# Kernel optimization log

Measured on AMD Instinct MI355X. Metric: run time of the kernel, lower is better.

Reference implementation:

```python
import jax, jax.numpy as jnp
import numpy as np

N_NODES = 1_000_000
N_UPD = 200_000
D_MEM = 172
D_MSG = 172


def setup_inputs() -> dict:
    key = jax.random.key(0)
    ks = jax.random.split(key, 8)
    memory = jax.random.normal(ks[0], (N_NODES, D_MEM), dtype=jnp.float32)
    last_update = jnp.zeros((N_NODES,), dtype=jnp.float32)
    # unique node ids (no duplicates, as guaranteed by the caller in the original code)
    unique_node_ids = jax.random.permutation(ks[1], N_NODES)[:N_UPD].astype(jnp.int64)
    unique_messages = jax.random.normal(ks[2], (N_UPD, D_MSG), dtype=jnp.float32)
    timestamps = jax.random.uniform(ks[3], (N_UPD,), dtype=jnp.float32) * 1e6
    s_ih = 1.0 / np.sqrt(D_MEM)
    weight_ih = jax.random.uniform(ks[4], (3 * D_MEM, D_MSG), jnp.float32, -s_ih, s_ih)
    weight_hh = jax.random.uniform(ks[5], (3 * D_MEM, D_MEM), jnp.float32, -s_ih, s_ih)
    bias_ih = jax.random.uniform(ks[6], (3 * D_MEM,), jnp.float32, -s_ih, s_ih)
    bias_hh = jax.random.uniform(ks[7], (3 * D_MEM,), jnp.float32, -s_ih, s_ih)
    return {
        "memory": memory,
        "last_update": last_update,
        "unique_node_ids": unique_node_ids,
        "unique_messages": unique_messages,
        "timestamps": timestamps,
        "weight_ih": weight_ih,
        "weight_hh": weight_hh,
        "bias_ih": bias_ih,
        "bias_hh": bias_hh,
    }


def _gru_cell(x, h, weight_ih, weight_hh, bias_ih, bias_hh):
    # PyTorch GRUCell, gate order: reset, update, new
    gi = x @ weight_ih.T + bias_ih          # [M, 3H]
    gh = h @ weight_hh.T + bias_hh          # [M, 3H]
    i_r, i_z, i_n = jnp.split(gi, 3, axis=-1)
    h_r, h_z, h_n = jnp.split(gh, 3, axis=-1)
    r = jax.nn.sigmoid(i_r + h_r)
    z = jax.nn.sigmoid(i_z + h_z)
    n = jnp.tanh(i_n + r * h_n)
    return n + z * (h - n)                  # (1-z)*n + z*h


def reference(memory, last_update, unique_node_ids, unique_messages, timestamps,
              weight_ih, weight_hh, bias_ih, bias_hh):
    # gather rows of the node memory for the updated nodes
    h = memory[unique_node_ids]                                   # [M, D]
    h_new = _gru_cell(unique_messages, h, weight_ih, weight_hh, bias_ih, bias_hh)
    # scatter updated rows back (ids are unique)
    updated_memory = memory.at[unique_node_ids].set(h_new)        # [N, D]
    updated_last_update = last_update.at[unique_node_ids].set(timestamps)
    # original module returns memory with the singleton middle dim restored
    return updated_memory[:, None, :], updated_last_update
```

## Files before the change

kernel.cpp:

```cpp
#include <hip/hip_runtime.h>

typedef __attribute__((ext_vector_type(8))) short short8;
typedef __attribute__((ext_vector_type(4))) float f32x4;

#define N_NODES 1000000
#define N_UPD   200000
#define D       172
#define BM      64
#define LDA     360
#define KSTEPS  11
#define NTILES  48
#define KSLICE  (NTILES*512)
#define GRU_TILES (N_UPD / BM)
#define GRID    512
#define SLAB4   13760
#define SLABLU  320
#define NM4     43000000
#define BPACK_USHORTS (KSTEPS*KSLICE)
#define BIAS_OFF  (BPACK_USHORTS*2)
#define MASK_OFF  (BIAS_OFF + 688*4)
#define WS_NEED   (MASK_OFF + N_NODES)

__device__ __forceinline__ unsigned short f2bf(float f) {
  union { float f; unsigned u; } v; v.f = f;
  unsigned r = v.u + 0x7FFFu + ((v.u >> 16) & 1u);
  return (unsigned short)(r >> 16);
}
__device__ __forceinline__ float bf2f(unsigned short h) {
  union { unsigned u; float f; } v; v.u = ((unsigned)h) << 16;
  return v.f;
}
__device__ __forceinline__ ushort4 f2bf4(float4 v) {
  return make_ushort4(f2bf(v.x), f2bf(v.y), f2bf(v.z), f2bf(v.w));
}

__global__ void prep_kernel(const float* __restrict__ wih, const float* __restrict__ whh,
                            const float* __restrict__ bih, const float* __restrict__ bhh,
                            unsigned short* __restrict__ Bpack, float* __restrict__ bias4,
                            uint4* __restrict__ mask16) {
  int gid = blockIdx.x * 256 + threadIdx.x;
  if (gid < 688) {
    int which = gid / 172, j = gid % 172;
    float v;
    if (which == 0)      v = bih[j]       + bhh[j];
    else if (which == 1) v = bih[172 + j] + bhh[172 + j];
    else if (which == 2) v = bih[344 + j];
    else                 v = bhh[344 + j];
    bias4[gid] = v;
  }
  if (gid < N_NODES / 16) mask16[gid] = make_uint4(0, 0, 0, 0);
  if (gid >= BPACK_USHORTS) return;
  int e  = gid & 7;
  int l  = (gid >> 3) & 63;
  int nt = (gid >> 9) % NTILES;
  int ks = gid / KSLICE;
  int k  = ks * 32 + ((l >> 4) << 3) + e;
  int c  = l & 15;
  int w  = nt / 12, tl = nt % 12;
  int gate = tl / 3, ti = tl % 3;
  int j = w * 48 + ti * 16 + c;
  float v = 0.f;
  if (j < D) {
    if (gate == 0) {
      if (k < D)        v = wih[j * D + k];
      else if (k < 2*D) v = whh[j * D + (k - D)];
    } else if (gate == 1) {
      if (k < D)        v = wih[(D + j) * D + k];
      else if (k < 2*D) v = whh[(D + j) * D + (k - D)];
    } else if (gate == 2) {
      if (k < D)        v = wih[(2*D + j) * D + k];
    } else {
      if (k >= D && k < 2*D) v = whh[(2*D + j) * D + (k - D)];
    }
  }
  Bpack[gid] = f2bf(v);
}

__global__ void mask_set_kernel(const int* __restrict__ ids, unsigned char* __restrict__ mask) {
  int i = blockIdx.x * 256 + threadIdx.x;
  if (i < N_UPD) mask[ids[i]] = 1;
}

__global__ void copy_kernel(const float4* __restrict__ mem4, const float4* __restrict__ lu4,
                            float4* __restrict__ out4, float4* __restrict__ outlu4) {
  const long NL4 = N_NODES / 4;
  long stride = (long)gridDim.x * blockDim.x;
  for (long i = (long)blockIdx.x * blockDim.x + threadIdx.x; i < NM4 + NL4; i += stride) {
    if (i < NM4) out4[i] = mem4[i];
    else         outlu4[i - NM4] = lu4[i - NM4];
  }
}

template<int HAS_COPY>
__global__ __launch_bounds__(512, 4)
void fused_kernel(const float* __restrict__ memory, const float* __restrict__ last_update,
                  const float* __restrict__ msgs, const int* __restrict__ ids,
                  const float* __restrict__ ts, const unsigned short* __restrict__ Bpack,
                  const float* __restrict__ bias4, const unsigned char* __restrict__ mask,
                  float* __restrict__ out_mem, float* __restrict__ out_lu) {
  __shared__ unsigned short At[BM * LDA];
  const int tid  = threadIdx.x;
  const int wave = tid >> 6, lane = tid & 63;
  const int g = lane >> 4, c = lane & 15;
  const int wm = wave >> 2, wc = wave & 3;
  const int ar0 = (wm * 32 + c) * LDA;
  const int ar1 = ar0 + 16 * LDA;
  const short8* Bp = (const short8*)Bpack;
  const float4* mem4 = (const float4*)memory;
  float4* out4 = (float4*)out_mem;

  for (int s = blockIdx.x; s < GRU_TILES; s += GRID) {
    const int m0 = s * BM;

    {
      const float4* x4 = (const float4*)msgs + (size_t)m0 * 43;
      float4 xv[6], hv[6];
      #pragma unroll
      for (int i = 0; i < 6; ++i) {
        int q = tid + i * 512;
        if (i < 5 || q < 2752) xv[i] = x4[q];
      }
      #pragma unroll
      for (int i = 0; i < 6; ++i) {
        int q = tid + i * 512;
        if (i < 5 || q < 2752) {
          int row = q / 43, seg = q - row * 43;
          hv[i] = ((const float4*)(memory + (size_t)ids[m0 + row] * D))[seg];
        }
      }
      #pragma unroll
      for (int i = 0; i < 6; ++i) {
        int q = tid + i * 512;
        if (i < 5 || q < 2752) {
          int row = q / 43, seg = q - row * 43;
          *(ushort4*)&At[row * LDA + seg * 4]       = f2bf4(xv[i]);
          *(ushort4*)&At[row * LDA + 172 + seg * 4] = f2bf4(hv[i]);
        }
      }
      if (tid < BM) {
        *(uint4*)&At[tid * LDA + 344] = make_uint4(0, 0, 0, 0);
        out_lu[ids[m0 + tid]] = ts[m0 + tid];
      }
    }
    __syncthreads();

    #pragma unroll 1
    for (int ti = 0; ti < 3; ++ti) {
      if (wc == 3 && ti == 2) continue;
      const short8* bp = Bp + (size_t)((wc * 12 + ti) * 64 + lane);

      f32x4 Cr0={0,0,0,0}, Cr1={0,0,0,0};
      f32x4 Cz0={0,0,0,0}, Cz1={0,0,0,0};
      f32x4 Ci0={0,0,0,0}, Ci1={0,0,0,0};
      f32x4 Ch0={0,0,0,0}, Ch1={0,0,0,0};

      #pragma unroll 2
      for (int ks = 0; ks < KSTEPS; ++ks) {
        short8 a0 = *(const short8*)&At[ar0 + ks * 32 + g * 8];
        short8 a1 = *(const short8*)&At[ar1 + ks * 32 + g * 8];
        const short8* bk = bp + ks * 3072;
        short8 br = bk[0];
        short8 bz = bk[192];
        short8 bi = bk[384];
        short8 bh = bk[576];
        Cr0 = __builtin_amdgcn_mfma_f32_16x16x32_bf16(a0, br, Cr0, 0, 0, 0);
        Cr1 = __builtin_amdgcn_mfma_f32_16x16x32_bf16(a1, br, Cr1, 0, 0, 0);
        Cz0 = __builtin_amdgcn_mfma_f32_16x16x32_bf16(a0, bz, Cz0, 0, 0, 0);
        Cz1 = __builtin_amdgcn_mfma_f32_16x16x32_bf16(a1, bz, Cz1, 0, 0, 0);
        Ci0 = __builtin_amdgcn_mfma_f32_16x16x32_bf16(a0, bi, Ci0, 0, 0, 0);
        Ci1 = __builtin_amdgcn_mfma_f32_16x16x32_bf16(a1, bi, Ci1, 0, 0, 0);
        Ch0 = __builtin_amdgcn_mfma_f32_16x16x32_bf16(a0, bh, Ch0, 0, 0, 0);
        Ch1 = __builtin_amdgcn_mfma_f32_16x16x32_bf16(a1, bh, Ch1, 0, 0, 0);
      }

      const int j = wc * 48 + ti * 16 + c;
      if (j < D) {
        const float b_r = bias4[j];
        const float b_z = bias4[172 + j];
        const float b_i = bias4[344 + j];
        const float b_h = bias4[516 + j];
        #pragma unroll
        for (int r = 0; r < 4; ++r) {
          {
            const int row_local = wm * 32 + g * 4 + r;
            float* orow = out_mem + (size_t)ids[m0 + row_local] * D;
            float ho = bf2f(At[row_local * LDA + 172 + j]);
            float rr = 1.f / (1.f + __expf(-(Cr0[r] + b_r)));
            float zz = 1.f / (1.f + __expf(-(Cz0[r] + b_z)));
            float e2 = __expf(2.f * (Ci0[r] + b_i + rr * (Ch0[r] + b_h)));
            float nn = 1.f - 2.f / (e2 + 1.f);
            orow[j] = nn + zz * (ho - nn);
          }
          {
            const int row_local = wm * 32 + 16 + g * 4 + r;
            float* orow = out_mem + (size_t)ids[m0 + row_local] * D;
            float ho = bf2f(At[row_local * LDA + 172 + j]);
            float rr = 1.f / (1.f + __expf(-(Cr1[r] + b_r)));
            float zz = 1.f / (1.f + __expf(-(Cz1[r] + b_z)));
            float e2 = __expf(2.f * (Ci1[r] + b_i + rr * (Ch1[r] + b_h)));
            float nn = 1.f - 2.f / (e2 + 1.f);
            orow[j] = nn + zz * (ho - nn);
          }
        }
      }
    }

    if (HAS_COPY) {
      const unsigned base = (unsigned)s * SLAB4;
      #pragma unroll 1
      for (int i = tid; i < SLAB4; i += 512) {
        unsigned idx = base + i;
        unsigned row = idx / 43u;
        if (!mask[row]) out4[idx] = mem4[idx];
      }
      if (tid < SLABLU) {
        unsigned jj = (unsigned)s * SLABLU + tid;
        if (!mask[jj]) out_lu[jj] = last_update[jj];
      }
    }
    __syncthreads();
  }
}

extern "C" void kernel_launch(void* const* d_in, const int* in_sizes, int n_in,
                              void* d_out, int out_size, void* d_ws, size_t ws_size,
                              hipStream_t stream) {
  const float* memory      = (const float*)d_in[0];
  const float* last_update = (const float*)d_in[1];
  const int*   ids         = (const int*)  d_in[2];
  const float* msgs        = (const float*)d_in[3];
  const float* ts          = (const float*)d_in[4];
  const float* wih         = (const float*)d_in[5];
  const float* whh         = (const float*)d_in[6];
  const float* bih         = (const float*)d_in[7];
  const float* bhh         = (const float*)d_in[8];

  float* out_mem = (float*)d_out;
  float* out_lu  = out_mem + (size_t)N_NODES * D;

  unsigned short* Bpack = (unsigned short*)d_ws;
  float* bias4 = (float*)((char*)d_ws + BIAS_OFF);
  unsigned char* mask = (unsigned char*)d_ws + MASK_OFF;

  prep_kernel<<<BPACK_USHORTS / 256, 256, 0, stream>>>(wih, whh, bih, bhh, Bpack, bias4,
                                                       (uint4*)mask);
  if (ws_size >= WS_NEED) {
    mask_set_kernel<<<(N_UPD + 255) / 256, 256, 0, stream>>>(ids, mask);
    fused_kernel<1><<<GRID, 512, 0, stream>>>(memory, last_update, msgs, ids, ts,
                                              Bpack, bias4, mask, out_mem, out_lu);
  } else {
    copy_kernel<<<4096, 256, 0, stream>>>((const float4*)memory, (const float4*)last_update,
                                          (float4*)out_mem, (float4*)out_lu);
    fused_kernel<0><<<GRID, 512, 0, stream>>>(memory, last_update, msgs, ids, ts,
                                              Bpack, bias4, mask, out_mem, out_lu);
  }
}
```

Measured before the change: 584.0 us.

## Launch one block per GRU tile and interleave copy loads with MFMA work

Replaces the persistent grid-stride loop (512 blocks) with one block per 64-row tile (3125 blocks). The non-updated memory copy for each block's slab is split into three chunks of 9 float4s per thread. Each chunk's loads are issued before that chunk's MFMA loop and stored after it, so copy latency can overlap the matrix work. This adds register pressure from holding 9 float4s plus mask bytes, which may lower occupancy under the launch bounds.

Measured after the change: 680.5 us. 16.5% more time.

```diff
diff --git a/kernel.cpp b/kernel.cpp
--- a/kernel.cpp
+++ b/kernel.cpp
@@ -11,10 +11,10 @@
 #define KSTEPS  11
 #define NTILES  48
 #define KSLICE  (NTILES*512)
-#define GRU_TILES (N_UPD / BM)
-#define GRID    512
+#define GRU_BLOCKS (N_UPD / BM)
 #define SLAB4   13760
 #define SLABLU  320
+#define CPT     9
 #define NM4     43000000
 #define BPACK_USHORTS (KSTEPS*KSLICE)
 #define BIAS_OFF  (BPACK_USHORTS*2)
@@ -93,67 +93,83 @@
 
 template<int HAS_COPY>
 __global__ __launch_bounds__(512, 4)
-void fused_kernel(const float* __restrict__ memory, const float* __restrict__ last_update,
+void gru64_kernel(const float* __restrict__ memory, const float* __restrict__ last_update,
                   const float* __restrict__ msgs, const int* __restrict__ ids,
                   const float* __restrict__ ts, const unsigned short* __restrict__ Bpack,
                   const float* __restrict__ bias4, const unsigned char* __restrict__ mask,
                   float* __restrict__ out_mem, float* __restrict__ out_lu) {
   __shared__ unsigned short At[BM * LDA];
   const int tid  = threadIdx.x;
+  const int m0   = blockIdx.x * BM;
   const int wave = tid >> 6, lane = tid & 63;
   const int g = lane >> 4, c = lane & 15;
   const int wm = wave >> 2, wc = wave & 3;
+  const float4* mem4 = (const float4*)memory;
+  float4* out4 = (float4*)out_mem;
+  const unsigned cbase = (unsigned)blockIdx.x * SLAB4 + tid;
+
+  {
+    const float4* x4 = (const float4*)msgs + (size_t)m0 * 43;
+    float4 xv[6], hv[6];
+    #pragma unroll
+    for (int i = 0; i < 6; ++i) {
+      int q = tid + i * 512;
+      if (i < 5 || q < 2752) xv[i] = x4[q];
+    }
+    #pragma unroll
+    for (int i = 0; i < 6; ++i) {
+      int q = tid + i * 512;
+      if (i < 5 || q < 2752) {
+        int row = q / 43, seg = q - row * 43;
+        hv[i] = ((const float4*)(memory + (size_t)ids[m0 + row] * D))[seg];
+      }
+    }
+    #pragma unroll
+    for (int i = 0; i < 6; ++i) {
+      int q = tid + i * 512;
+      if (i < 5 || q < 2752) {
+        int row = q / 43, seg = q - row * 43;
+        *(ushort4*)&At[row * LDA + seg * 4]       = f2bf4(xv[i]);
+        *(ushort4*)&At[row * LDA + 172 + seg * 4] = f2bf4(hv[i]);
+      }
+    }
+    if (tid < BM) {
+      *(uint4*)&At[tid * LDA + 344] = make_uint4(0, 0, 0, 0);
+      out_lu[ids[m0 + tid]] = ts[m0 + tid];
+    }
+    if (HAS_COPY && tid < SLABLU) {
+      unsigned jj = (unsigned)blockIdx.x * SLABLU + tid;
+      if (!mask[jj]) out_lu[jj] = last_update[jj];
+    }
+  }
+  __syncthreads();
+
   const int ar0 = (wm * 32 + c) * LDA;
   const int ar1 = ar0 + 16 * LDA;
   const short8* Bp = (const short8*)Bpack;
-  const float4* mem4 = (const float4*)memory;
-  float4* out4 = (float4*)out_mem;
-
-  for (int s = blockIdx.x; s < GRU_TILES; s += GRID) {
-    const int m0 = s * BM;
-
-    {
-      const float4* x4 = (const float4*)msgs + (size_t)m0 * 43;
-      float4 xv[6], hv[6];
+
+  #pragma unroll 1
+  for (int ti = 0; ti < 3; ++ti) {
+    float4 cv[CPT]; unsigned char cm[CPT];
+    if (HAS_COPY) {
       #pragma unroll
-      for (int i = 0; i < 6; ++i) {
-        int q = tid + i * 512;
-        if (i < 5 || q < 2752) xv[i] = x4[q];
-      }
-      #pragma unroll
-      for (int i = 0; i < 6; ++i) {
-        int q = tid + i * 512;
-        if (i < 5 || q < 2752) {
-          int row = q / 43, seg = q - row * 43;
-          hv[i] = ((const float4*)(memory + (size_t)ids[m0 + row] * D))[seg];
-        }
-      }
-      #pragma unroll
-      for (int i = 0; i < 6; ++i) {
-        int q = tid + i * 512;
-        if (i < 5 || q < 2752) {
-          int row = q / 43, seg = q - row * 43;
-          *(ushort4*)&At[row * LDA + seg * 4]       = f2bf4(xv[i]);
-          *(ushort4*)&At[row * LDA + 172 + seg * 4] = f2bf4(hv[i]);
-        }
-      }
-      if (tid < BM) {
-        *(uint4*)&At[tid * LDA + 344] = make_uint4(0, 0, 0, 0);
-        out_lu[ids[m0 + tid]] = ts[m0 + tid];
-      }
-    }
-    __syncthreads();
-
-    #pragma unroll 1
-    for (int ti = 0; ti < 3; ++ti) {
-      if (wc == 3 && ti == 2) continue;
+      for (int i = 0; i < CPT; ++i) {
+        unsigned idx = cbase + (unsigned)(ti * CPT + i) * 512;
+        if (idx < NM4) {
+          cv[i] = mem4[idx];
+          cm[i] = mask[idx / 43u];
+        } else cm[i] = 1;
+      }
+    }
+
+    const bool live = !(wc == 3 && ti == 2);
+    f32x4 Cr0={0,0,0,0}, Cr1={0,0,0,0};
+    f32x4 Cz0={0,0,0,0}, Cz1={0,0,0,0};
+    f32x4 Ci0={0,0,0,0}, Ci1={0,0,0,0};
+    f32x4 Ch0={0,0,0,0}, Ch1={0,0,0,0};
+
+    if (live) {
       const short8* bp = Bp + (size_t)((wc * 12 + ti) * 64 + lane);
-
-      f32x4 Cr0={0,0,0,0}, Cr1={0,0,0,0};
-      f32x4 Cz0={0,0,0,0}, Cz1={0,0,0,0};
-      f32x4 Ci0={0,0,0,0}, Ci1={0,0,0,0};
-      f32x4 Ch0={0,0,0,0}, Ch1={0,0,0,0};
-
       #pragma unroll 2
       for (int ks = 0; ks < KSTEPS; ++ks) {
         short8 a0 = *(const short8*)&At[ar0 + ks * 32 + g * 8];
@@ -172,7 +188,17 @@
         Ch0 = __builtin_amdgcn_mfma_f32_16x16x32_bf16(a0, bh, Ch0, 0, 0, 0);
         Ch1 = __builtin_amdgcn_mfma_f32_16x16x32_bf16(a1, bh, Ch1, 0, 0, 0);
       }
-
+    }
+
+    if (HAS_COPY) {
+      #pragma unroll
+      for (int i = 0; i < CPT; ++i) {
+        unsigned idx = cbase + (unsigned)(ti * CPT + i) * 512;
+        if (idx < NM4 && !cm[i]) out4[idx] = cv[i];
+      }
+    }
+
+    if (live) {
       const int j = wc * 48 + ti * 16 + c;
       if (j < D) {
         const float b_r = bias4[j];
@@ -204,21 +230,6 @@
         }
       }
     }
-
-    if (HAS_COPY) {
-      const unsigned base = (unsigned)s * SLAB4;
-      #pragma unroll 1
-      for (int i = tid; i < SLAB4; i += 512) {
-        unsigned idx = base + i;
-        unsigned row = idx / 43u;
-        if (!mask[row]) out4[idx] = mem4[idx];
-      }
-      if (tid < SLABLU) {
-        unsigned jj = (unsigned)s * SLABLU + tid;
-        if (!mask[jj]) out_lu[jj] = last_update[jj];
-      }
-    }
-    __syncthreads();
   }
 }
 
@@ -246,12 +257,12 @@
                                                        (uint4*)mask);
   if (ws_size >= WS_NEED) {
     mask_set_kernel<<<(N_UPD + 255) / 256, 256, 0, stream>>>(ids, mask);
-    fused_kernel<1><<<GRID, 512, 0, stream>>>(memory, last_update, msgs, ids, ts,
-                                              Bpack, bias4, mask, out_mem, out_lu);
+    gru64_kernel<1><<<GRU_BLOCKS, 512, 0, stream>>>(memory, last_update, msgs, ids, ts,
+                                                    Bpack, bias4, mask, out_mem, out_lu);
   } else {
     copy_kernel<<<4096, 256, 0, stream>>>((const float4*)memory, (const float4*)last_update,
                                           (float4*)out_mem, (float4*)out_lu);
-    fused_kernel<0><<<GRID, 512, 0, stream>>>(memory, last_update, msgs, ids, ts,
-                                              Bpack, bias4, mask, out_mem, out_lu);
-  }
-}
+    gru64_kernel<0><<<GRU_BLOCKS, 512, 0, stream>>>(memory, last_update, msgs, ids, ts,
+                                                    Bpack, bias4, mask, out_mem, out_lu);
+  }
+}
```

## Warp-specialize fused GRU kernel: dedicated copy waves, one tile per block

Applied to the files above, without the earlier changes.

Replaces the persistent grid-stride loop with one 64-row tile per block and grows each block to 768 threads. The first 512 threads load, convert and run the MFMA GRU, while the extra 256 threads stream the masked memory-copy slab for that tile. The goal is to overlap the bandwidth-bound copy with the MFMA and gather work instead of running them back to back inside each block. In exchange the larger block is limited by launch_bounds(768,6), which may cap registers or occupancy, and the copy waves must still wait at the barrier until the tile load finishes.

Measured after the change: 625.4 us. +7.1%, slower.

```diff
diff --git a/kernel.cpp b/kernel.cpp
--- a/kernel.cpp
+++ b/kernel.cpp
@@ -11,8 +11,7 @@
 #define KSTEPS  11
 #define NTILES  48
 #define KSLICE  (NTILES*512)
-#define GRU_TILES (N_UPD / BM)
-#define GRID    512
+#define GRU_BLOCKS (N_UPD / BM)
 #define SLAB4   13760
 #define SLABLU  320
 #define NM4     43000000
@@ -92,133 +91,138 @@
 }
 
 template<int HAS_COPY>
-__global__ __launch_bounds__(512, 4)
+__global__ __launch_bounds__(768, 6)
 void fused_kernel(const float* __restrict__ memory, const float* __restrict__ last_update,
                   const float* __restrict__ msgs, const int* __restrict__ ids,
                   const float* __restrict__ ts, const unsigned short* __restrict__ Bpack,
                   const float* __restrict__ bias4, const unsigned char* __restrict__ mask,
                   float* __restrict__ out_mem, float* __restrict__ out_lu) {
   __shared__ unsigned short At[BM * LDA];
-  const int tid  = threadIdx.x;
+  const int tid = threadIdx.x;
+  const int m0  = blockIdx.x * BM;
+
+  if (tid < 512) {
+    const float4* x4 = (const float4*)msgs + (size_t)m0 * 43;
+    #pragma unroll
+    for (int p = 0; p < 2; ++p) {
+      float4 xv[3], hv[3];
+      #pragma unroll
+      for (int i = 0; i < 3; ++i) {
+        int q = tid + (p * 3 + i) * 512;
+        if (p == 0 || i < 2 || q < 2752) xv[i] = x4[q];
+      }
+      #pragma unroll
+      for (int i = 0; i < 3; ++i) {
+        int q = tid + (p * 3 + i) * 512;
+        if (p == 0 || i < 2 || q < 2752) {
+          int row = q / 43, seg = q - row * 43;
+          hv[i] = ((const float4*)(memory + (size_t)ids[m0 + row] * D))[seg];
+        }
+      }
+      #pragma unroll
+      for (int i = 0; i < 3; ++i) {
+        int q = tid + (p * 3 + i) * 512;
+        if (p == 0 || i < 2 || q < 2752) {
+          int row = q / 43, seg = q - row * 43;
+          *(ushort4*)&At[row * LDA + seg * 4]       = f2bf4(xv[i]);
+          *(ushort4*)&At[row * LDA + 172 + seg * 4] = f2bf4(hv[i]);
+        }
+      }
+    }
+    if (tid < BM) {
+      *(uint4*)&At[tid * LDA + 344] = make_uint4(0, 0, 0, 0);
+      out_lu[ids[m0 + tid]] = ts[m0 + tid];
+    }
+  }
+  __syncthreads();
+
+  if (tid >= 512) {
+    if (HAS_COPY) {
+      const int ct = tid - 512;
+      const float4* mem4 = (const float4*)memory;
+      float4* out4 = (float4*)out_mem;
+      const unsigned base = (unsigned)blockIdx.x * SLAB4;
+      #pragma unroll 1
+      for (int i = ct; i < SLAB4; i += 256) {
+        unsigned idx = base + i;
+        unsigned row = idx / 43u;
+        if (!mask[row]) out4[idx] = mem4[idx];
+      }
+      #pragma unroll 1
+      for (int i = ct; i < SLABLU; i += 256) {
+        unsigned jj = (unsigned)blockIdx.x * SLABLU + i;
+        if (!mask[jj]) out_lu[jj] = last_update[jj];
+      }
+    }
+    return;
+  }
+
   const int wave = tid >> 6, lane = tid & 63;
   const int g = lane >> 4, c = lane & 15;
   const int wm = wave >> 2, wc = wave & 3;
   const int ar0 = (wm * 32 + c) * LDA;
   const int ar1 = ar0 + 16 * LDA;
   const short8* Bp = (const short8*)Bpack;
-  const float4* mem4 = (const float4*)memory;
-  float4* out4 = (float4*)out_mem;
-
-  for (int s = blockIdx.x; s < GRU_TILES; s += GRID) {
-    const int m0 = s * BM;
-
-    {
-      const float4* x4 = (const float4*)msgs + (size_t)m0 * 43;
-      float4 xv[6], hv[6];
-      #pragma unroll
-      for (int i = 0; i < 6; ++i) {
-        int q = tid + i * 512;
-        if (i < 5 || q < 2752) xv[i] = x4[q];
-      }
-      #pragma unroll
-      for (int i = 0; i < 6; ++i) {
-        int q = tid + i * 512;
-        if (i < 5 || q < 2752) {
-          int row = q / 43, seg = q - row * 43;
-          hv[i] = ((const float4*)(memory + (size_t)ids[m0 + row] * D))[seg];
-        }
-      }
-      #pragma unroll
-      for (int i = 0; i < 6; ++i) {
-        int q = tid + i * 512;
-        if (i < 5 || q < 2752) {
-          int row = q / 43, seg = q - row * 43;
-          *(ushort4*)&At[row * LDA + seg * 4]       = f2bf4(xv[i]);
-          *(ushort4*)&At[row * LDA + 172 + seg * 4] = f2bf4(hv[i]);
-        }
-      }
-      if (tid < BM) {
-        *(uint4*)&At[tid * LDA + 344] = make_uint4(0, 0, 0, 0);
-        out_lu[ids[m0 + tid]] = ts[m0 + tid];
-      }
-    }
-    __syncthreads();
-
-    #pragma unroll 1
-    for (int ti = 0; ti < 3; ++ti) {
-      if (wc == 3 && ti == 2) continue;
-      const short8* bp = Bp + (size_t)((wc * 12 + ti) * 64 + lane);
-
-      f32x4 Cr0={0,0,0,0}, Cr1={0,0,0,0};
-      f32x4 Cz0={0,0,0,0}, Cz1={0,0,0,0};
-      f32x4 Ci0={0,0,0,0}, Ci1={0,0,0,0};
-      f32x4 Ch0={0,0,0,0}, Ch1={0,0,0,0};
-
-      #pragma unroll 2
-      for (int ks = 0; ks < KSTEPS; ++ks) {
-        short8 a0 = *(const short8*)&At[ar0 + ks * 32 + g * 8];
-        short8 a1 = *(const short8*)&At[ar1 + ks * 32 + g * 8];
-        const short8* bk = bp + ks * 3072;
-        short8 br = bk[0];
-        short8 bz = bk[192];
-        short8 bi = bk[384];
-        short8 bh = bk[576];
-        Cr0 = __builtin_amdgcn_mfma_f32_16x16x32_bf16(a0, br, Cr0, 0, 0, 0);
-        Cr1 = __builtin_amdgcn_mfma_f32_16x16x32_bf16(a1, br, Cr1, 0, 0, 0);
-        Cz0 = __builtin_amdgcn_mfma_f32_16x16x32_bf16(a0, bz, Cz0, 0, 0, 0);
-        Cz1 = __builtin_amdgcn_mfma_f32_16x16x32_bf16(a1, bz, Cz1, 0, 0, 0);
-        Ci0 = __builtin_amdgcn_mfma_f32_16x16x32_bf16(a0, bi, Ci0, 0, 0, 0);
-        Ci1 = __builtin_amdgcn_mfma_f32_16x16x32_bf16(a1, bi, Ci1, 0, 0, 0);
-        Ch0 = __builtin_amdgcn_mfma_f32_16x16x32_bf16(a0, bh, Ch0, 0, 0, 0);
-        Ch1 = __builtin_amdgcn_mfma_f32_16x16x32_bf16(a1, bh, Ch1, 0, 0, 0);
-      }
-
-      const int j = wc * 48 + ti * 16 + c;
-      if (j < D) {
-        const float b_r = bias4[j];
-        const float b_z = bias4[172 + j];
-        const float b_i = bias4[344 + j];
-        const float b_h = bias4[516 + j];
-        #pragma unroll
-        for (int r = 0; r < 4; ++r) {
-          {
-            const int row_local = wm * 32 + g * 4 + r;
-            float* orow = out_mem + (size_t)ids[m0 + row_local] * D;
-            float ho = bf2f(At[row_local * LDA + 172 + j]);
-            float rr = 1.f / (1.f + __expf(-(Cr0[r] + b_r)));
-            float zz = 1.f / (1.f + __expf(-(Cz0[r] + b_z)));
-            float e2 = __expf(2.f * (Ci0[r] + b_i + rr * (Ch0[r] + b_h)));
-            float nn = 1.f - 2.f / (e2 + 1.f);
-            orow[j] = nn + zz * (ho - nn);
-          }
-          {
-            const int row_local = wm * 32 + 16 + g * 4 + r;
-            float* orow = out_mem + (size_t)ids[m0 + row_local] * D;
-            float ho = bf2f(At[row_local * LDA + 172 + j]);
-            float rr = 1.f / (1.f + __expf(-(Cr1[r] + b_r)));
-            float zz = 1.f / (1.f + __expf(-(Cz1[r] + b_z)));
-            float e2 = __expf(2.f * (Ci1[r] + b_i + rr * (Ch1[r] + b_h)));
-            float nn = 1.f - 2.f / (e2 + 1.f);
-            orow[j] = nn + zz * (ho - nn);
-          }
-        }
-      }
-    }
-
-    if (HAS_COPY) {
-      const unsigned base = (unsigned)s * SLAB4;
-      #pragma unroll 1
-      for (int i = tid; i < SLAB4; i += 512) {
-        unsigned idx = base + i;
-        unsigned row = idx / 43u;
-        if (!mask[row]) out4[idx] = mem4[idx];
-      }
-      if (tid < SLABLU) {
-        unsigned jj = (unsigned)s * SLABLU + tid;
-        if (!mask[jj]) out_lu[jj] = last_update[jj];
-      }
-    }
-    __syncthreads();
+
+  #pragma unroll 1
+  for (int ti = 0; ti < 3; ++ti) {
+    if (wc == 3 && ti == 2) continue;
+    const short8* bp = Bp + (size_t)((wc * 12 + ti) * 64 + lane);
+
+    f32x4 Cr0={0,0,0,0}, Cr1={0,0,0,0};
+    f32x4 Cz0={0,0,0,0}, Cz1={0,0,0,0};
+    f32x4 Ci0={0,0,0,0}, Ci1={0,0,0,0};
+    f32x4 Ch0={0,0,0,0}, Ch1={0,0,0,0};
+
+    #pragma unroll 2
+    for (int ks = 0; ks < KSTEPS; ++ks) {
+      short8 a0 = *(const short8*)&At[ar0 + ks * 32 + g * 8];
+      short8 a1 = *(const short8*)&At[ar1 + ks * 32 + g * 8];
+      const short8* bk = bp + ks * 3072;
+      short8 br = bk[0];
+      short8 bz = bk[192];
+      short8 bi = bk[384];
+      short8 bh = bk[576];
+      Cr0 = __builtin_amdgcn_mfma_f32_16x16x32_bf16(a0, br, Cr0, 0, 0, 0);
+      Cr1 = __builtin_amdgcn_mfma_f32_16x16x32_bf16(a1, br, Cr1, 0, 0, 0);
+      Cz0 = __builtin_amdgcn_mfma_f32_16x16x32_bf16(a0, bz, Cz0, 0, 0, 0);
+      Cz1 = __builtin_amdgcn_mfma_f32_16x16x32_bf16(a1, bz, Cz1, 0, 0, 0);
+      Ci0 = __builtin_amdgcn_mfma_f32_16x16x32_bf16(a0, bi, Ci0, 0, 0, 0);
+      Ci1 = __builtin_amdgcn_mfma_f32_16x16x32_bf16(a1, bi, Ci1, 0, 0, 0);
+      Ch0 = __builtin_amdgcn_mfma_f32_16x16x32_bf16(a0, bh, Ch0, 0, 0, 0);
+      Ch1 = __builtin_amdgcn_mfma_f32_16x16x32_bf16(a1, bh, Ch1, 0, 0, 0);
+    }
+
+    const int j = wc * 48 + ti * 16 + c;
+    if (j < D) {
+      const float b_r = bias4[j];
+      const float b_z = bias4[172 + j];
+      const float b_i = bias4[344 + j];
+      const float b_h = bias4[516 + j];
+      #pragma unroll
+      for (int r = 0; r < 4; ++r) {
+        {
+          const int row_local = wm * 32 + g * 4 + r;
+          float* orow = out_mem + (size_t)ids[m0 + row_local] * D;
+          float ho = bf2f(At[row_local * LDA + 172 + j]);
+          float rr = 1.f / (1.f + __expf(-(Cr0[r] + b_r)));
+          float zz = 1.f / (1.f + __expf(-(Cz0[r] + b_z)));
+          float e2 = __expf(2.f * (Ci0[r] + b_i + rr * (Ch0[r] + b_h)));
+          float nn = 1.f - 2.f / (e2 + 1.f);
+          orow[j] = nn + zz * (ho - nn);
+        }
+        {
+          const int row_local = wm * 32 + 16 + g * 4 + r;
+          float* orow = out_mem + (size_t)ids[m0 + row_local] * D;
+          float ho = bf2f(At[row_local * LDA + 172 + j]);
+          float rr = 1.f / (1.f + __expf(-(Cr1[r] + b_r)));
+          float zz = 1.f / (1.f + __expf(-(Cz1[r] + b_z)));
+          float e2 = __expf(2.f * (Ci1[r] + b_i + rr * (Ch1[r] + b_h)));
+          float nn = 1.f - 2.f / (e2 + 1.f);
+          orow[j] = nn + zz * (ho - nn);
+        }
+      }
+    }
   }
 }
 
@@ -246,12 +250,12 @@
                                                        (uint4*)mask);
   if (ws_size >= WS_NEED) {
     mask_set_kernel<<<(N_UPD + 255) / 256, 256, 0, stream>>>(ids, mask);
-    fused_kernel<1><<<GRID, 512, 0, stream>>>(memory, last_update, msgs, ids, ts,
-                                              Bpack, bias4, mask, out_mem, out_lu);
+    fused_kernel<1><<<GRU_BLOCKS, 768, 0, stream>>>(memory, last_update, msgs, ids, ts,
+                                                    Bpack, bias4, mask, out_mem, out_lu);
   } else {
     copy_kernel<<<4096, 256, 0, stream>>>((const float4*)memory, (const float4*)last_update,
                                           (float4*)out_mem, (float4*)out_lu);
-    fused_kernel<0><<<GRID, 512, 0, stream>>>(memory, last_update, msgs, ids, ts,
-                                              Bpack, bias4, mask, out_mem, out_lu);
-  }
-}
+    fused_kernel<0><<<GRU_BLOCKS, 768, 0, stream>>>(memory, last_update, msgs, ids, ts,
+                                                    Bpack, bias4, mask, out_mem, out_lu);
+  }
+}
```
